# Performance work log

Measured on AMD Instinct MI355X. Metric: run time of the kernel, lower is better.

The kernel has to match this reference:

```python
import jax, jax.numpy as jnp
import numpy as np

N = 12288
E = 393216
H = 128
NEG = -1000000000.0

def setup_inputs() -> dict:
    key = jax.random.key(0)
    k1, k2, k3, k4, k5, k6 = jax.random.split(key, 6)
    h = jax.random.normal(k1, (N, H), dtype=jnp.float32)
    sources = jax.random.randint(k2, (E,), 0, N, dtype=jnp.int32)
    dests = jax.random.randint(k3, (E,), 0, N, dtype=jnp.int32)
    weights = jax.random.normal(k4, (E, 1), dtype=jnp.float32)
    # nn.Linear(2*H+1, 1) params
    W = jax.random.normal(k5, (1, 2 * H + 1), dtype=jnp.float32) / np.sqrt(2 * H + 1)
    b = jax.random.normal(k6, (1,), dtype=jnp.float32) * 0.01
    return {"h": h, "sources": sources, "dests": dests, "weights": weights, "W": W, "b": b}

def reference(h, sources, dests, weights, W, b):
    n = h.shape[0]
    # gather endpoint features and concat with edge weights: [E, 2H+1]
    edge_input = jnp.concatenate([h[dests], h[sources], weights], axis=1)
    vals = (edge_input @ W.T + b)[:, 0]  # [E]
    scores = jnp.full((n, n), NEG, dtype=h.dtype)
    scores = scores.at[dests, sources].set(vals)
    return scores
```

## Files before the change

### kernel.cpp

```cpp
#include <hip/hip_runtime.h>

#define NEG_VAL -1000000000.0f

__global__ __launch_bounds__(256) void fill_and_dots(
    float4* __restrict__ out4,
    long long n4,
    int fillBlocks,
    const float* __restrict__ h,
    const float* __restrict__ W,
    float* __restrict__ a,
    float* __restrict__ c,
    int N)
{
    if ((int)blockIdx.x < fillBlocks) {
        long long i = (long long)blockIdx.x * 256 + threadIdx.x;
        if (i < n4) {
            out4[i] = make_float4(NEG_VAL, NEG_VAL, NEG_VAL, NEG_VAL);
        }
    } else {
        int gid  = (blockIdx.x - fillBlocks) * 256 + threadIdx.x;
        int node = gid >> 6;
        int lane = threadIdx.x & 63;
        if (node >= N) return;

        const float2* h2 = (const float2*)(h + (size_t)node * 128);
        float2 v  = h2[lane];
        float2 wd = ((const float2*)W)[lane];
        float2 ws = ((const float2*)(W + 128))[lane];

        float sd = v.x * wd.x + v.y * wd.y;
        float ss = v.x * ws.x + v.y * ws.y;

        #pragma unroll
        for (int off = 32; off; off >>= 1) {
            sd += __shfl_xor(sd, off, 64);
            ss += __shfl_xor(ss, off, 64);
        }
        if (lane == 0) {
            a[node] = sd;
            c[node] = ss;
        }
    }
}

__global__ __launch_bounds__(256) void edge_scatter(
    const int* __restrict__ src,
    const int* __restrict__ dst,
    const float* __restrict__ wgt,
    const float* __restrict__ a,
    const float* __restrict__ c,
    const float* __restrict__ W,
    const float* __restrict__ b,
    float* __restrict__ out,
    int E, int N)
{
    int e = blockIdx.x * blockDim.x + threadIdx.x;
    if (e >= E) return;
    int s = src[e];
    int d = dst[e];
    float val = fmaf(wgt[e], W[256], a[d] + c[s] + b[0]);
    out[(size_t)d * N + s] = val;
}

extern "C" void kernel_launch(void* const* d_in, const int* in_sizes, int n_in,
                              void* d_out, int out_size, void* d_ws, size_t ws_size,
                              hipStream_t stream) {
    const float* h       = (const float*)d_in[0];
    const int*   sources = (const int*)d_in[1];
    const int*   dests   = (const int*)d_in[2];
    const float* weights = (const float*)d_in[3];
    const float* W       = (const float*)d_in[4];
    const float* b       = (const float*)d_in[5];
    float* out = (float*)d_out;

    const int N = in_sizes[0] / 128;
    const int E = in_sizes[1];

    float* a = (float*)d_ws;
    float* c = a + N;

    {
        long long n4 = (long long)out_size / 4;
        int fillBlocks = (int)((n4 + 255) / 256);
        int dotBlocks  = (N + 3) / 4;
        fill_and_dots<<<fillBlocks + dotBlocks, 256, 0, stream>>>(
            (float4*)out, n4, fillBlocks, h, W, a, c, N);
    }

    {
        int blocks = (E + 255) / 256;
        edge_scatter<<<blocks, 256, 0, stream>>>(sources, dests, weights, a, c, W, b,
                                                 out, E, N);
    }
}
```

Baseline: 628.3 us.

## Bucket edges by destination row and write output rows with patches fused in

Replaces the full-matrix fill followed by a random per-edge scatter. Edges are first bucketed by destination row into a fixed-capacity (192 per row) buffer using atomic cursors. A fill kernel then writes each 1024-column row segment exactly once, with coalesced float4 stores, inserting that segment's edge values from shared memory. This removes the scattered partial-line writes into the 600 MB output. In exchange it adds a bucketing pass, a workspace requirement of about 19 MB, and a redundant scan of each row's edges by every segment block. It also silently drops edges beyond 192 per row, and when several edges share a cell the winning value depends on atomic ordering.

```diff
diff --git a/kernel.cpp b/kernel.cpp
--- a/kernel.cpp
+++ b/kernel.cpp
@@ -1,65 +1,135 @@
 #include <hip/hip_runtime.h>
 
 #define NEG_VAL -1000000000.0f
+#define MAXDEG  192
+#define SEGF    1024
+
 
 __global__ __launch_bounds__(256) void fill_and_dots(
-    float4* __restrict__ out4,
-    long long n4,
-    int fillBlocks,
-    const float* __restrict__ h,
-    const float* __restrict__ W,
-    float* __restrict__ a,
-    float* __restrict__ c,
-    int N)
+    float4* __restrict__ out4, long long n4, int fillBlocks,
+    const float* __restrict__ h, const float* __restrict__ W,
+    float* __restrict__ a, float* __restrict__ c, int N)
 {
     if ((int)blockIdx.x < fillBlocks) {
         long long i = (long long)blockIdx.x * 256 + threadIdx.x;
-        if (i < n4) {
-            out4[i] = make_float4(NEG_VAL, NEG_VAL, NEG_VAL, NEG_VAL);
-        }
+        if (i < n4) out4[i] = make_float4(NEG_VAL, NEG_VAL, NEG_VAL, NEG_VAL);
     } else {
         int gid  = (blockIdx.x - fillBlocks) * 256 + threadIdx.x;
         int node = gid >> 6;
         int lane = threadIdx.x & 63;
         if (node >= N) return;
-
         const float2* h2 = (const float2*)(h + (size_t)node * 128);
         float2 v  = h2[lane];
         float2 wd = ((const float2*)W)[lane];
         float2 ws = ((const float2*)(W + 128))[lane];
-
         float sd = v.x * wd.x + v.y * wd.y;
         float ss = v.x * ws.x + v.y * ws.y;
-
         #pragma unroll
         for (int off = 32; off; off >>= 1) {
             sd += __shfl_xor(sd, off, 64);
             ss += __shfl_xor(ss, off, 64);
         }
-        if (lane == 0) {
-            a[node] = sd;
-            c[node] = ss;
-        }
+        if (lane == 0) { a[node] = sd; c[node] = ss; }
     }
 }
 
 __global__ __launch_bounds__(256) void edge_scatter(
-    const int* __restrict__ src,
-    const int* __restrict__ dst,
-    const float* __restrict__ wgt,
-    const float* __restrict__ a,
-    const float* __restrict__ c,
-    const float* __restrict__ W,
-    const float* __restrict__ b,
-    float* __restrict__ out,
-    int E, int N)
+    const int* __restrict__ src, const int* __restrict__ dst,
+    const float* __restrict__ wgt, const float* __restrict__ a,
+    const float* __restrict__ c, const float* __restrict__ W,
+    const float* __restrict__ b, float* __restrict__ out, int E, int N)
 {
     int e = blockIdx.x * blockDim.x + threadIdx.x;
     if (e >= E) return;
     int s = src[e];
     int d = dst[e];
-    float val = fmaf(wgt[e], W[256], a[d] + c[s] + b[0]);
-    out[(size_t)d * N + s] = val;
+    out[(size_t)d * N + s] = fmaf(wgt[e], W[256], a[d] + c[s] + b[0]);
+}
+
+
+__global__ __launch_bounds__(256) void zero_cursor(int* __restrict__ cursor, int N) {
+    int i = blockIdx.x * 256 + threadIdx.x;
+    if (i < N) cursor[i] = 0;
+}
+
+__global__ __launch_bounds__(256) void dots_and_emit(
+    const float* __restrict__ h, const float* __restrict__ W,
+    float* __restrict__ a, float* __restrict__ c, int N,
+    const int* __restrict__ src, const int* __restrict__ dst,
+    const float* __restrict__ wgt,
+    int* __restrict__ cursor, int2* __restrict__ csr, int E, int dotBlocks)
+{
+    if ((int)blockIdx.x < dotBlocks) {
+        int gid  = blockIdx.x * 256 + threadIdx.x;
+        int node = gid >> 6;
+        int lane = threadIdx.x & 63;
+        if (node >= N) return;
+        const float2* h2 = (const float2*)(h + (size_t)node * 128);
+        float2 v  = h2[lane];
+        float2 wd = ((const float2*)W)[lane];
+        float2 ws = ((const float2*)(W + 128))[lane];
+        float sd = v.x * wd.x + v.y * wd.y;
+        float ss = v.x * ws.x + v.y * ws.y;
+        #pragma unroll
+        for (int off = 32; off; off >>= 1) {
+            sd += __shfl_xor(sd, off, 64);
+            ss += __shfl_xor(ss, off, 64);
+        }
+        if (lane == 0) { a[node] = sd; c[node] = ss; }
+    } else {
+        int e = (blockIdx.x - dotBlocks) * 256 + threadIdx.x;
+        if (e >= E) return;
+        int d = dst[e];
+        int slot = atomicAdd(&cursor[d], 1);
+        if (slot < MAXDEG)
+            csr[(size_t)d * MAXDEG + slot] = make_int2(src[e], __float_as_int(wgt[e]));
+    }
+}
+
+__global__ __launch_bounds__(256) void fill_patch(
+    float4* __restrict__ out4,
+    const float* __restrict__ a, const float* __restrict__ c,
+    const int* __restrict__ cursor, const int2* __restrict__ csr,
+    const float* __restrict__ W, const float* __restrict__ b, int N)
+{
+    __shared__ int   pcol[256];
+    __shared__ float pval[256];
+    __shared__ int   pcnt;
+
+    int seg        = blockIdx.x;
+    int segsPerRow = N >> 10;
+    int r          = seg / segsPerRow;
+    int colBase    = (seg - r * segsPerRow) << 10;
+    int tid        = threadIdx.x;
+
+    if (tid == 0) pcnt = 0;
+    __syncthreads();
+
+    int   cnt  = min(cursor[r], MAXDEG);
+    float w256 = W[256];
+    float bb   = b[0];
+    float ar   = a[r];
+
+    for (int i = tid; i < cnt; i += 256) {
+        int2 eo  = csr[(size_t)r * MAXDEG + i];
+        int  rel = eo.x - colBase;
+        if ((unsigned)rel < SEGF) {
+            int k = atomicAdd(&pcnt, 1);
+            if (k < 256) {
+                pcol[k] = rel;
+                pval[k] = fmaf(__int_as_float(eo.y), w256, ar + c[eo.x] + bb);
+            }
+        }
+    }
+    __syncthreads();
+
+    float4 v = make_float4(NEG_VAL, NEG_VAL, NEG_VAL, NEG_VAL);
+    int m = min(pcnt, 256);
+    for (int k = 0; k < m; ++k) {
+        int rel = pcol[k];
+        if ((rel >> 2) == tid) ((float*)&v)[rel & 3] = pval[k];
+    }
+    out4[(size_t)seg * (SEGF / 4) + tid] = v;
 }
 
 extern "C" void kernel_launch(void* const* d_in, const int* in_sizes, int n_in,
@@ -76,18 +146,29 @@
     const int N = in_sizes[0] / 128;
     const int E = in_sizes[1];
 
-    float* a = (float*)d_ws;
-    float* c = a + N;
+    float* a      = (float*)d_ws;
+    float* c      = a + N;
+    int*   cursor = (int*)(c + N);
+    int2*  csr    = (int2*)(cursor + N);
+    size_t wsNeed = (size_t)N * 12 + (size_t)N * MAXDEG * 8;
 
-    {
+    if ((N % 1024) == 0 && ws_size >= wsNeed) {
+        zero_cursor<<<(N + 255) / 256, 256, 0, stream>>>(cursor, N);
+
+        int dotBlocks  = N / 4;
+        int emitBlocks = (E + 255) / 256;
+        dots_and_emit<<<dotBlocks + emitBlocks, 256, 0, stream>>>(
+            h, W, a, c, N, sources, dests, weights, cursor, csr, E, dotBlocks);
+
+        int nseg = (N >> 10) * N;
+        fill_patch<<<nseg, 256, 0, stream>>>(
+            (float4*)out, a, c, cursor, csr, W, b, N);
+    } else {
         long long n4 = (long long)out_size / 4;
         int fillBlocks = (int)((n4 + 255) / 256);
         int dotBlocks  = (N + 3) / 4;
         fill_and_dots<<<fillBlocks + dotBlocks, 256, 0, stream>>>(
             (float4*)out, n4, fillBlocks, h, W, a, c, N);
-    }
-
-    {
         int blocks = (E + 255) / 256;
         edge_scatter<<<blocks, 256, 0, stream>>>(sources, dests, weights, a, c, W, b,
                                                  out, E, N);
```

New measurement: 714.1 us. 1.14x slower.
